# Kernel tuning notes

Measured on AMD Instinct MI355X. Metric: run time of the kernel, lower is better.

## Reference

```python
import jax, jax.numpy as jnp
import numpy as np

IN_DIM = 512
HID = 1024
E = 16
TOPK = 2


def setup_inputs() -> dict:
    key = jax.random.key(0)
    ks = jax.random.split(key, 8)
    s = 0.02
    x = jax.random.normal(ks[0], (4, 2048, IN_DIM), dtype=jnp.float32)
    Wr = jax.random.normal(ks[1], (IN_DIM, E), dtype=jnp.float32) * s
    br = jnp.zeros((E,), dtype=jnp.float32)
    W1 = jax.random.normal(ks[2], (E, IN_DIM, HID), dtype=jnp.float32) * s
    b1 = jnp.zeros((E, HID), dtype=jnp.float32)
    W2 = jax.random.normal(ks[3], (E, HID, IN_DIM), dtype=jnp.float32) * s
    b2 = jnp.zeros((E, IN_DIM), dtype=jnp.float32)
    return {"x": x, "Wr": Wr, "br": br, "W1": W1, "b1": b1, "W2": W2, "b2": b2}


def reference(x, Wr, br, W1, b1, W2, b2):
    token_shape = x.shape[:-1]
    xf = x.reshape(-1, x.shape[-1])            # [T, D]
    T = xf.shape[0]

    # router (temperature = 1.0)
    logits = xf @ Wr + br                       # [T, E]
    probs = jax.nn.softmax(logits, axis=-1)
    topk_w, topk_idx = jax.lax.top_k(probs, TOPK)           # [T, K]
    topk_w = topk_w / jnp.maximum(topk_w.sum(-1, keepdims=True), 1e-9)

    # combine weights: [T, E], zero where not routed
    combine = jnp.zeros((T, E), dtype=xf.dtype).at[
        jnp.arange(T)[:, None], topk_idx].add(topk_w)

    # per-expert MLP (exact GELU, as torch nn.GELU default), weighted combine
    y = jnp.zeros_like(xf)
    for e in range(E):
        h = jax.nn.gelu(xf @ W1[e] + b1[e], approximate=False)  # [T, H]
        o = h @ W2[e] + b2[e]                                   # [T, D]
        y = y + combine[:, e:e + 1] * o

    # residual (in_dim == out_dim)
    y = xf + y
    return y.reshape(*token_shape, IN_DIM)
```

## Files before the change

kernel.cpp:

```cpp
#include <hip/hip_runtime.h>
#include <hip/hip_bf16.h>
#include <math.h>

#define IN_DIM 512
#define HID    1024
#define NE     16
#define T_TOK  8192
#define NPAIR  (T_TOK*2)

typedef __attribute__((ext_vector_type(8))) short bf16x8;
typedef __attribute__((ext_vector_type(4))) float f32x4;

__device__ __forceinline__ unsigned short f2b(float f){
  unsigned u = __float_as_uint(f);
  u += 0x7FFF + ((u >> 16) & 1);
  return (unsigned short)(u >> 16);
}
__device__ __forceinline__ float b2f(unsigned short u){
  return __uint_as_float(((unsigned)u) << 16);
}

__global__ __launch_bounds__(256) void tconv_kernel(const float* __restrict__ in,
                                                    unsigned short* __restrict__ out,
                                                    int M, int N){
  __shared__ float tile[32][33];
  int e  = blockIdx.z;
  int m0 = blockIdx.y*32, n0 = blockIdx.x*32;
  const float* src = in + (size_t)e*M*N;
  unsigned short* dst = out + (size_t)e*M*N;
  int c = threadIdx.x & 31, r = threadIdx.x >> 5;
  #pragma unroll
  for (int i=0;i<4;i++)
    tile[r + i*8][c] = src[(size_t)(m0 + r + i*8)*N + n0 + c];
  __syncthreads();
  int tr  = threadIdx.x >> 3;
  int tc4 = (threadIdx.x & 7) * 4;
  ushort4 o;
  o.x = f2b(tile[tc4+0][tr]); o.y = f2b(tile[tc4+1][tr]);
  o.z = f2b(tile[tc4+2][tr]); o.w = f2b(tile[tc4+3][tr]);
  *(ushort4*)(&dst[(size_t)(n0 + tr)*M + m0 + tc4]) = o;
}

__global__ __launch_bounds__(256) void router_kernel(
    const float* __restrict__ x, const float* __restrict__ Wr, const float* __restrict__ br,
    unsigned short* __restrict__ xb, int* __restrict__ eid, float* __restrict__ pw)
{
  int wid = threadIdx.x >> 6, lane = threadIdx.x & 63;
  int t = blockIdx.x*4 + wid;
  const float4* xr4 = (const float4*)(x + (size_t)t*IN_DIM);
  ushort4*      xb4 = (ushort4*)(xb + (size_t)t*IN_DIM);

  float acc[NE];
  #pragma unroll
  for (int i=0;i<NE;i++) acc[i]=0.f;

  #pragma unroll
  for (int j=0;j<2;j++){
    int f = j*64 + lane;
    float4 v = xr4[f];
    ushort4 o; o.x=f2b(v.x); o.y=f2b(v.y); o.z=f2b(v.z); o.w=f2b(v.w);
    xb4[f] = o;
    const float4* wr4 = (const float4*)(Wr + (size_t)(f*4)*NE);
    const float* vv = (const float*)&v;
    #pragma unroll
    for (int rr=0; rr<4; rr++){
      float xv = vv[rr];
      #pragma unroll
      for (int q=0;q<4;q++){
        float4 w = wr4[rr*4+q];
        acc[q*4+0] += xv*w.x; acc[q*4+1] += xv*w.y;
        acc[q*4+2] += xv*w.z; acc[q*4+3] += xv*w.w;
      }
    }
  }
  #pragma unroll
  for (int off=32; off>=1; off>>=1){
    #pragma unroll
    for (int i=0;i<NE;i++) acc[i] += __shfl_xor(acc[i], off, 64);
  }
  if (lane==0){
    #pragma unroll
    for (int i=0;i<NE;i++) acc[i] += br[i];
    int e0=0; float l0=acc[0];
    #pragma unroll
    for (int i=1;i<NE;i++) if (acc[i] > l0){ l0=acc[i]; e0=i; }
    int e1=-1; float l1=-3.0e38f;
    #pragma unroll
    for (int i=0;i<NE;i++) if (i!=e0 && acc[i] > l1){ l1=acc[i]; e1=i; }
    float w0 = 1.f/(1.f + __expf(l1 - l0));
    float w1 = 1.f - w0;
    pw[t*2+0] = w0; pw[t*2+1] = w1;
    eid[t*2+0] = e0; eid[t*2+1] = e1;
  }
}

__global__ __launch_bounds__(1024) void bucket_kernel(const int* __restrict__ eid,
                                                      int* __restrict__ cnt,
                                                      int* __restrict__ bucket){
  int e = blockIdx.x;
  __shared__ int lbase;
  if (threadIdx.x == 0) lbase = 0;
  __syncthreads();
  int lane = threadIdx.x & 63, wid = threadIdx.x >> 6;
  int* be = bucket + e*T_TOK;
  for (int c = wid*64; c < NPAIR; c += 1024){
    int p = c + lane;
    bool ok = (eid[p] == e);
    unsigned long long m = __ballot(ok);
    int rank = __popcll(m & ((1ull << lane) - 1ull));
    int count = __popcll(m);
    int base = 0;
    if (lane == 0) base = atomicAdd(&lbase, count);
    base = __shfl(base, 0, 64);
    if (ok) be[base + rank] = p;
  }
  __syncthreads();
  if (threadIdx.x == 0) cnt[e] = lbase;
}

template<int KDIM, int NDIM, bool FIRST>
__global__ __launch_bounds__(256) void moe_gemm(
    const unsigned short* __restrict__ A,
    const unsigned short* __restrict__ Bm,
    const float* __restrict__ bias,
    const int* __restrict__ cnt,
    const int* __restrict__ bucket,
    const float* __restrict__ pw,
    unsigned short* __restrict__ hb,
    unsigned short* __restrict__ opb)
{
  int e  = blockIdx.z;
  int n0 = blockIdx.x * 128;
  int i0 = blockIdx.y * 64;
  int ce = cnt[e];
  if (i0 >= ce) return;

  __shared__ unsigned short As[64][40];
  __shared__ unsigned short Bs[128][40];

  int tid = threadIdx.x;
  int lane = tid & 63, wid = tid >> 6;
  int wm = (wid>>1)*32, wn = (wid&1)*64;

  int lr0 = tid >> 2;
  int lc  = (tid & 3) * 8;
  const int* buck = bucket + e*T_TOK;
  int posA  = i0 + lr0;
  int pairA = (posA < ce) ? buck[posA] : buck[i0];
  size_t arow = (size_t)(FIRST ? (pairA >> 1) : pairA) * KDIM + lc;
  const unsigned short* Bp = Bm + (size_t)e*NDIM*KDIM + (size_t)(n0 + lr0)*KDIM + lc;

  f32x4 acc[2][4];
  #pragma unroll
  for (int a=0;a<2;a++)
    #pragma unroll
    for (int b=0;b<4;b++)
      #pragma unroll
      for (int j=0;j<4;j++) acc[a][b][j] = 0.f;

  for (int k0 = 0; k0 < KDIM; k0 += 32){
    float4 av = *(const float4*)(A + arow + k0);
    float4 bv0 = *(const float4*)(Bp + k0);
    float4 bv1 = *(const float4*)(Bp + (size_t)64*KDIM + k0);
    *(float4*)(&As[lr0][lc]) = av;
    *(float4*)(&Bs[lr0][lc]) = bv0;
    *(float4*)(&Bs[lr0+64][lc]) = bv1;
    __syncthreads();
    int fr = lane & 15, fo = (lane>>4)*8;
    bf16x8 af[2], bfr[4];
    #pragma unroll
    for (int s=0;s<2;s++) af[s]  = *(const bf16x8*)(&As[wm + s*16 + fr][fo]);
    #pragma unroll
    for (int u=0;u<4;u++) bfr[u] = *(const bf16x8*)(&Bs[wn + u*16 + fr][fo]);
    #pragma unroll
    for (int s=0;s<2;s++)
      #pragma unroll
      for (int u=0;u<4;u++)
        acc[s][u] = __builtin_amdgcn_mfma_f32_16x16x32_bf16(af[s], bfr[u], acc[s][u], 0,0,0);
    __syncthreads();
  }

  int fr = lane & 15, fq = (lane>>4)*4;
  #pragma unroll
  for (int s=0;s<2;s++){
    #pragma unroll
    for (int i=0;i<4;i++){
      int row = wm + s*16 + fq + i;
      int pos = i0 + row;
      if (pos >= ce) continue;
      int pair = buck[pos];
      float w = FIRST ? 0.f : pw[pair];
      #pragma unroll
      for (int u=0;u<4;u++){
        int n = n0 + wn + u*16 + fr;
        float v = acc[s][u][i] + bias[e*NDIM + n];
        if (FIRST){
          float g = 0.5f*v*(1.f + erff(v*0.70710678118654752f));
          hb[(size_t)pair*NDIM + n] = f2b(g);
        } else {
          opb[(size_t)pair*NDIM + n] = f2b(w*v);
        }
      }
    }
  }
}

__global__ __launch_bounds__(256) void combine_kernel(const float* __restrict__ x,
                                                      const unsigned short* __restrict__ opb,
                                                      float* __restrict__ out){
  int i = blockIdx.x*256 + threadIdx.x;
  int t  = i >> 7;
  int c4 = i & 127;
  float4 v = ((const float4*)x)[i];
  ushort4 a = ((const ushort4*)opb)[(size_t)(2*t)*128 + c4];
  ushort4 b = ((const ushort4*)opb)[(size_t)(2*t+1)*128 + c4];
  v.x += b2f(a.x) + b2f(b.x);
  v.y += b2f(a.y) + b2f(b.y);
  v.z += b2f(a.z) + b2f(b.z);
  v.w += b2f(a.w) + b2f(b.w);
  ((float4*)out)[i] = v;
}

extern "C" void kernel_launch(void* const* d_in, const int* in_sizes, int n_in,
                              void* d_out, int out_size, void* d_ws, size_t ws_size,
                              hipStream_t stream)
{
  const float* x  = (const float*)d_in[0];
  const float* Wr = (const float*)d_in[1];
  const float* br = (const float*)d_in[2];
  const float* W1 = (const float*)d_in[3];
  const float* b1 = (const float*)d_in[4];
  const float* W2 = (const float*)d_in[5];
  const float* b2 = (const float*)d_in[6];
  float* out = (float*)d_out;
  char* ws = (char*)d_ws;

  int*            cnt    = (int*)(ws + 0);
  int*            bucket = (int*)(ws + 1024);
  float*          pw     = (float*)(ws + 525312);
  unsigned short* xb     = (unsigned short*)(ws + 590848);
  unsigned short* w1t    = (unsigned short*)(ws + 8979456);
  unsigned short* w2t    = (unsigned short*)(ws + 25756672);
  unsigned short* hb     = (unsigned short*)(ws + 42533888);
  int*            eid    = (int*)(ws + 42533888);
  unsigned short* opb    = w1t;

  router_kernel<<<T_TOK/4, 256, 0, stream>>>(x, Wr, br, xb, eid, pw);
  bucket_kernel<<<NE, 1024, 0, stream>>>(eid, cnt, bucket);
  tconv_kernel<<<dim3(HID/32, IN_DIM/32, NE), 256, 0, stream>>>(W1, w1t, IN_DIM, HID);
  tconv_kernel<<<dim3(IN_DIM/32, HID/32, NE), 256, 0, stream>>>(W2, w2t, HID, IN_DIM);
  moe_gemm<IN_DIM, HID, true ><<<dim3(HID/128,    T_TOK/64, NE), 256, 0, stream>>>(
      xb, w1t, b1, cnt, bucket, pw, hb, opb);
  moe_gemm<HID, IN_DIM, false><<<dim3(IN_DIM/128, T_TOK/64, NE), 256, 0, stream>>>(
      hb, w2t, b2, cnt, bucket, pw, hb, opb);
  combine_kernel<<<(T_TOK*IN_DIM/4)/256, 256, 0, stream>>>(x, opb, out);
}
```

Measured before the change: 285.3 us.

## Double-buffer LDS tiles with register prefetch and XOR-swizzled layout in MoE GEMM

Rewrites the MoE GEMM main loop to use two LDS buffers and keep the next tile in registers. Global loads for step k+2 and LDS stores for step k+1 overlap with the MFMAs on step k, and only one barrier is needed per iteration. The padded [rows][40] layout becomes an unpadded 32-wide layout with an XOR swizzle on 16-byte chunks to avoid bank conflicts. This uses more registers and a little more LDS, which may lower occupancy.

```diff
diff --git a/kernel.cpp b/kernel.cpp
--- a/kernel.cpp
+++ b/kernel.cpp
@@ -134,21 +134,24 @@
   int i0 = blockIdx.y * 64;
   int ce = cnt[e];
   if (i0 >= ce) return;
-
-  __shared__ unsigned short As[64][40];
-  __shared__ unsigned short Bs[128][40];
+  constexpr int NS = KDIM / 32;
+
+  __shared__ unsigned short As[2*64*32];
+  __shared__ unsigned short Bs[2*128*32];
 
   int tid = threadIdx.x;
   int lane = tid & 63, wid = tid >> 6;
   int wm = (wid>>1)*32, wn = (wid&1)*64;
 
   int lr0 = tid >> 2;
-  int lc  = (tid & 3) * 8;
+  int c   = tid & 3;
+  int sc  = (c ^ ((lr0 >> 1) & 3)) * 8;
+  int wA  = lr0*32 + sc;
   const int* buck = bucket + e*T_TOK;
   int posA  = i0 + lr0;
   int pairA = (posA < ce) ? buck[posA] : buck[i0];
-  size_t arow = (size_t)(FIRST ? (pairA >> 1) : pairA) * KDIM + lc;
-  const unsigned short* Bp = Bm + (size_t)e*NDIM*KDIM + (size_t)(n0 + lr0)*KDIM + lc;
+  const unsigned short* Ag = A + (size_t)(FIRST ? (pairA >> 1) : pairA) * KDIM + c*8;
+  const unsigned short* Bg = Bm + (size_t)e*NDIM*KDIM + (size_t)(n0 + lr0)*KDIM + c*8;
 
   f32x4 acc[2][4];
   #pragma unroll
@@ -158,20 +161,45 @@
       #pragma unroll
       for (int j=0;j<4;j++) acc[a][b][j] = 0.f;
 
-  for (int k0 = 0; k0 < KDIM; k0 += 32){
-    float4 av = *(const float4*)(A + arow + k0);
-    float4 bv0 = *(const float4*)(Bp + k0);
-    float4 bv1 = *(const float4*)(Bp + (size_t)64*KDIM + k0);
-    *(float4*)(&As[lr0][lc]) = av;
-    *(float4*)(&Bs[lr0][lc]) = bv0;
-    *(float4*)(&Bs[lr0+64][lc]) = bv1;
-    __syncthreads();
-    int fr = lane & 15, fo = (lane>>4)*8;
+  int fr = lane & 15, fb = lane >> 4;
+  int pf8 = (fb ^ ((fr >> 1) & 3)) * 8;
+
+  float4 ar, br0, br1;
+  ar  = *(const float4*)(Ag);
+  br0 = *(const float4*)(Bg);
+  br1 = *(const float4*)(Bg + (size_t)64*KDIM);
+  *(float4*)(As + wA) = ar;
+  *(float4*)(Bs + wA) = br0;
+  *(float4*)(Bs + wA + 64*32) = br1;
+  ar  = *(const float4*)(Ag + 32);
+  br0 = *(const float4*)(Bg + 32);
+  br1 = *(const float4*)(Bg + (size_t)64*KDIM + 32);
+  __syncthreads();
+
+  #pragma unroll 2
+  for (int k = 0; k < NS; k++){
+    const int cur = k & 1, nxt = cur ^ 1;
+    float4 na, nb0, nb1;
+    bool ld = (k + 2 < NS);
+    if (ld){
+      na  = *(const float4*)(Ag + (k+2)*32);
+      nb0 = *(const float4*)(Bg + (k+2)*32);
+      nb1 = *(const float4*)(Bg + (size_t)64*KDIM + (k+2)*32);
+    }
+    if (k + 1 < NS){
+      *(float4*)(As + nxt*2048 + wA) = ar;
+      *(float4*)(Bs + nxt*4096 + wA) = br0;
+      *(float4*)(Bs + nxt*4096 + wA + 64*32) = br1;
+    }
+    if (ld){ ar = na; br0 = nb0; br1 = nb1; }
+
+    const unsigned short* Ac = As + cur*2048;
+    const unsigned short* Bc = Bs + cur*4096;
     bf16x8 af[2], bfr[4];
     #pragma unroll
-    for (int s=0;s<2;s++) af[s]  = *(const bf16x8*)(&As[wm + s*16 + fr][fo]);
-    #pragma unroll
-    for (int u=0;u<4;u++) bfr[u] = *(const bf16x8*)(&Bs[wn + u*16 + fr][fo]);
+    for (int s=0;s<2;s++) af[s]  = *(const bf16x8*)(Ac + (wm + s*16 + fr)*32 + pf8);
+    #pragma unroll
+    for (int u=0;u<4;u++) bfr[u] = *(const bf16x8*)(Bc + (wn + u*16 + fr)*32 + pf8);
     #pragma unroll
     for (int s=0;s<2;s++)
       #pragma unroll
@@ -180,7 +208,7 @@
     __syncthreads();
   }
 
-  int fr = lane & 15, fq = (lane>>4)*4;
+  int fq = (lane>>4)*4;
   #pragma unroll
   for (int s=0;s<2;s++){
     #pragma unroll
```

Measured after the change: 285.2 us. No clear change (-0.0%).

## Pack weights into MFMA fragment layout and load operands directly to registers

Applied to the files above, without the earlier changes.

Replaces the weight transpose with a packing kernel that writes W1/W2 in per-lane MFMA fragment order, so each lane reads its B fragment with one contiguous 16-byte load. The expert GEMM drops shared-memory staging and barriers and loads A and B fragments straight from global memory into registers, double-buffered in registers two K-steps ahead. This removes LDS traffic and syncs but gives up cross-wave reuse within a block, so each wave fetches its own A and B data and relies on cache for the sharing. The gathered A rows are read as scattered 16-byte loads.

```diff
diff --git a/kernel.cpp b/kernel.cpp
--- a/kernel.cpp
+++ b/kernel.cpp
@@ -20,25 +20,20 @@
   return __uint_as_float(((unsigned)u) << 16);
 }
 
-__global__ __launch_bounds__(256) void tconv_kernel(const float* __restrict__ in,
+__global__ __launch_bounds__(256) void packw_kernel(const float* __restrict__ in,
                                                     unsigned short* __restrict__ out,
-                                                    int M, int N){
-  __shared__ float tile[32][33];
-  int e  = blockIdx.z;
-  int m0 = blockIdx.y*32, n0 = blockIdx.x*32;
-  const float* src = in + (size_t)e*M*N;
-  unsigned short* dst = out + (size_t)e*M*N;
-  int c = threadIdx.x & 31, r = threadIdx.x >> 5;
-  #pragma unroll
-  for (int i=0;i<4;i++)
-    tile[r + i*8][c] = src[(size_t)(m0 + r + i*8)*N + n0 + c];
-  __syncthreads();
-  int tr  = threadIdx.x >> 3;
-  int tc4 = (threadIdx.x & 7) * 4;
-  ushort4 o;
-  o.x = f2b(tile[tc4+0][tr]); o.y = f2b(tile[tc4+1][tr]);
-  o.z = f2b(tile[tc4+2][tr]); o.w = f2b(tile[tc4+3][tr]);
-  *(ushort4*)(&dst[(size_t)(n0 + tr)*M + m0 + tc4]) = o;
+                                                    int K, int N){
+  int e  = blockIdx.z, nb = blockIdx.y;
+  int kb = blockIdx.x*4 + (threadIdx.x >> 6);
+  int l  = threadIdx.x & 63;
+  int KB = K/32, NB = N/16;
+  const float* src = in + (size_t)e*K*N + (size_t)(kb*32 + (l>>4)*8)*N + nb*16 + (l&15);
+  unsigned short o[8];
+  #pragma unroll
+  for (int j=0;j<8;j++) o[j] = f2b(src[(size_t)j*N]);
+  unsigned short* dst = out + (((size_t)e*NB + nb)*KB + kb)*512 + l*8;
+  *(ushort4*)(dst)   = *(ushort4*)(o);
+  *(ushort4*)(dst+4) = *(ushort4*)(o+4);
 }
 
 __global__ __launch_bounds__(256) void router_kernel(
@@ -121,7 +116,7 @@
 template<int KDIM, int NDIM, bool FIRST>
 __global__ __launch_bounds__(256) void moe_gemm(
     const unsigned short* __restrict__ A,
-    const unsigned short* __restrict__ Bm,
+    const unsigned short* __restrict__ Bp_,
     const float* __restrict__ bias,
     const int* __restrict__ cnt,
     const int* __restrict__ bucket,
@@ -129,26 +124,32 @@
     unsigned short* __restrict__ hb,
     unsigned short* __restrict__ opb)
 {
+  constexpr int KB = KDIM/32, NB = NDIM/16;
   int e  = blockIdx.z;
   int n0 = blockIdx.x * 128;
   int i0 = blockIdx.y * 64;
   int ce = cnt[e];
   if (i0 >= ce) return;
 
-  __shared__ unsigned short As[64][40];
-  __shared__ unsigned short Bs[128][40];
-
   int tid = threadIdx.x;
   int lane = tid & 63, wid = tid >> 6;
   int wm = (wid>>1)*32, wn = (wid&1)*64;
-
-  int lr0 = tid >> 2;
-  int lc  = (tid & 3) * 8;
+  int fr = lane & 15, fq8 = (lane>>4)*8;
   const int* buck = bucket + e*T_TOK;
-  int posA  = i0 + lr0;
-  int pairA = (posA < ce) ? buck[posA] : buck[i0];
-  size_t arow = (size_t)(FIRST ? (pairA >> 1) : pairA) * KDIM + lc;
-  const unsigned short* Bp = Bm + (size_t)e*NDIM*KDIM + (size_t)(n0 + lr0)*KDIM + lc;
+
+  const unsigned short* aP[2];
+  #pragma unroll
+  for (int s=0;s<2;s++){
+    int pos  = i0 + wm + s*16 + fr;
+    int pair = (pos < ce) ? buck[pos] : buck[i0];
+    int row  = FIRST ? (pair >> 1) : pair;
+    aP[s] = A + (size_t)row*KDIM + fq8;
+  }
+  const unsigned short* bP[4];
+  int nb0 = (n0 + wn) >> 4;
+  #pragma unroll
+  for (int u=0;u<4;u++)
+    bP[u] = Bp_ + (((size_t)e*NB + nb0 + u)*KB)*512 + lane*8;
 
   f32x4 acc[2][4];
   #pragma unroll
@@ -158,29 +159,56 @@
       #pragma unroll
       for (int j=0;j<4;j++) acc[a][b][j] = 0.f;
 
-  for (int k0 = 0; k0 < KDIM; k0 += 32){
-    float4 av = *(const float4*)(A + arow + k0);
-    float4 bv0 = *(const float4*)(Bp + k0);
-    float4 bv1 = *(const float4*)(Bp + (size_t)64*KDIM + k0);
-    *(float4*)(&As[lr0][lc]) = av;
-    *(float4*)(&Bs[lr0][lc]) = bv0;
-    *(float4*)(&Bs[lr0+64][lc]) = bv1;
-    __syncthreads();
-    int fr = lane & 15, fo = (lane>>4)*8;
-    bf16x8 af[2], bfr[4];
-    #pragma unroll
-    for (int s=0;s<2;s++) af[s]  = *(const bf16x8*)(&As[wm + s*16 + fr][fo]);
-    #pragma unroll
-    for (int u=0;u<4;u++) bfr[u] = *(const bf16x8*)(&Bs[wn + u*16 + fr][fo]);
+  bf16x8 a0[2], a1[2], b0[4], b1[4];
+  #pragma unroll
+  for (int s=0;s<2;s++){ a0[s] = *(const bf16x8*)(aP[s]);
+                         a1[s] = *(const bf16x8*)(aP[s] + 32); }
+  #pragma unroll
+  for (int u=0;u<4;u++){ b0[u] = *(const bf16x8*)(bP[u]);
+                         b1[u] = *(const bf16x8*)(bP[u] + 512); }
+
+  #pragma unroll 2
+  for (int k = 0; k < KB; k += 2){
+    bf16x8 ta[2], tb[4];
+    bool ld0 = (k+2) < KB;
+    if (ld0){
+      #pragma unroll
+      for (int s=0;s<2;s++) ta[s] = *(const bf16x8*)(aP[s] + (k+2)*32);
+      #pragma unroll
+      for (int u=0;u<4;u++) tb[u] = *(const bf16x8*)(bP[u] + (size_t)(k+2)*512);
+    }
     #pragma unroll
     for (int s=0;s<2;s++)
       #pragma unroll
       for (int u=0;u<4;u++)
-        acc[s][u] = __builtin_amdgcn_mfma_f32_16x16x32_bf16(af[s], bfr[u], acc[s][u], 0,0,0);
-    __syncthreads();
-  }
-
-  int fr = lane & 15, fq = (lane>>4)*4;
+        acc[s][u] = __builtin_amdgcn_mfma_f32_16x16x32_bf16(a0[s], b0[u], acc[s][u], 0,0,0);
+    if (ld0){
+      #pragma unroll
+      for (int s=0;s<2;s++) a0[s] = ta[s];
+      #pragma unroll
+      for (int u=0;u<4;u++) b0[u] = tb[u];
+    }
+    bool ld1 = (k+3) < KB;
+    if (ld1){
+      #pragma unroll
+      for (int s=0;s<2;s++) ta[s] = *(const bf16x8*)(aP[s] + (k+3)*32);
+      #pragma unroll
+      for (int u=0;u<4;u++) tb[u] = *(const bf16x8*)(bP[u] + (size_t)(k+3)*512);
+    }
+    #pragma unroll
+    for (int s=0;s<2;s++)
+      #pragma unroll
+      for (int u=0;u<4;u++)
+        acc[s][u] = __builtin_amdgcn_mfma_f32_16x16x32_bf16(a1[s], b1[u], acc[s][u], 0,0,0);
+    if (ld1){
+      #pragma unroll
+      for (int s=0;s<2;s++) a1[s] = ta[s];
+      #pragma unroll
+      for (int u=0;u<4;u++) b1[u] = tb[u];
+    }
+  }
+
+  int fq = (lane>>4)*4;
   #pragma unroll
   for (int s=0;s<2;s++){
     #pragma unroll
@@ -239,19 +267,19 @@
   int*            bucket = (int*)(ws + 1024);
   float*          pw     = (float*)(ws + 525312);
   unsigned short* xb     = (unsigned short*)(ws + 590848);
-  unsigned short* w1t    = (unsigned short*)(ws + 8979456);
-  unsigned short* w2t    = (unsigned short*)(ws + 25756672);
+  unsigned short* w1p    = (unsigned short*)(ws + 8979456);
+  unsigned short* w2p    = (unsigned short*)(ws + 25756672);
   unsigned short* hb     = (unsigned short*)(ws + 42533888);
   int*            eid    = (int*)(ws + 42533888);
-  unsigned short* opb    = w1t;
+  unsigned short* opb    = w1p;
 
   router_kernel<<<T_TOK/4, 256, 0, stream>>>(x, Wr, br, xb, eid, pw);
   bucket_kernel<<<NE, 1024, 0, stream>>>(eid, cnt, bucket);
-  tconv_kernel<<<dim3(HID/32, IN_DIM/32, NE), 256, 0, stream>>>(W1, w1t, IN_DIM, HID);
-  tconv_kernel<<<dim3(IN_DIM/32, HID/32, NE), 256, 0, stream>>>(W2, w2t, HID, IN_DIM);
+  packw_kernel<<<dim3(16/4, 64, NE), 256, 0, stream>>>(W1, w1p, IN_DIM, HID);
+  packw_kernel<<<dim3(32/4, 32, NE), 256, 0, stream>>>(W2, w2p, HID, IN_DIM);
   moe_gemm<IN_DIM, HID, true ><<<dim3(HID/128,    T_TOK/64, NE), 256, 0, stream>>>(
-      xb, w1t, b1, cnt, bucket, pw, hb, opb);
+      xb, w1p, b1, cnt, bucket, pw, hb, opb);
   moe_gemm<HID, IN_DIM, false><<<dim3(IN_DIM/128, T_TOK/64, NE), 256, 0, stream>>>(
-      hb, w2t, b2, cnt, bucket, pw, hb, opb);
+      hb, w2p, b2, cnt, bucket, pw, hb, opb);
   combine_kernel<<<(T_TOK*IN_DIM/4)/256, 256, 0, stream>>>(x, opb, out);
 }
```

Result: slower. 335.7 us (+17.7%).
